# Kernel optimization log

Measured on AMD Instinct MI355X. Metric: run time of the kernel, lower is better.

The kernel has to match this reference:

```python
import jax, jax.numpy as jnp
import numpy as np

N_QUBITS = 4
N_LAYERS = 3
DIM = 2 ** N_QUBITS  # 16


def _apply_1q_const(state, U, w):
    # state: (B, 16) complex64; U: (2, 2) constant gate on wire w (wire 0 = most significant)
    B = state.shape[0]
    left, right = 2 ** w, 2 ** (N_QUBITS - w - 1)
    s = state.reshape(B, left, 2, right)
    s = jnp.einsum('ij,bajc->baic', U, s)
    return s.reshape(B, DIM)


def _apply_1q_batched(state, U, w):
    # U: (B, 2, 2) per-sample gate (data re-uploading RY angles)
    B = state.shape[0]
    left, right = 2 ** w, 2 ** (N_QUBITS - w - 1)
    s = state.reshape(B, left, 2, right)
    s = jnp.einsum('bij,bajc->baic', U, s)
    return s.reshape(B, DIM)


def _cnot(state, c, t):
    # flip target axis amplitudes where control == 1
    B = state.shape[0]
    s = state.reshape((B,) + (2,) * N_QUBITS)
    s = jnp.moveaxis(s, (1 + c, 1 + t), (N_QUBITS - 1, N_QUBITS))
    s = s.at[..., 1, :].set(s[..., 1, ::-1])
    s = jnp.moveaxis(s, (N_QUBITS - 1, N_QUBITS), (1 + c, 1 + t))
    return s.reshape(B, DIM)


def _ry_batched(theta):
    # (B,) -> (B, 2, 2) RY matrices (real, cast to complex)
    c, s = jnp.cos(theta / 2), jnp.sin(theta / 2)
    return jnp.stack([jnp.stack([c, -s], -1), jnp.stack([s, c], -1)], -2).astype(jnp.complex64)


def _rot(phi, theta, omega):
    # PennyLane Rot = RZ(omega) RY(theta) RZ(phi)
    c, s = jnp.cos(theta / 2), jnp.sin(theta / 2)
    row0 = jnp.stack([jnp.exp(-1j * (phi + omega) / 2) * c, -jnp.exp(1j * (phi - omega) / 2) * s])
    row1 = jnp.stack([jnp.exp(-1j * (phi - omega) / 2) * s, jnp.exp(1j * (phi + omega) / 2) * c])
    return jnp.stack([row0, row1]).astype(jnp.complex64)


def _circuit(angles, q_weights):
    # angles: (B, 4); q_weights: (3, 4, 3). Returns <Z_0> per sample, (B,)
    B = angles.shape[0]
    state = jnp.zeros((B, DIM), jnp.complex64).at[:, 0].set(1.0)
    for l in range(N_LAYERS):
        # AngleEmbedding(rotation='Y') — same inputs re-uploaded each layer
        for w in range(N_QUBITS):
            state = _apply_1q_batched(state, _ry_batched(angles[:, w]), w)
        # StronglyEntanglingLayers, single layer -> range r = 1
        for w in range(N_QUBITS):
            phi, theta, omega = q_weights[l, w, 0], q_weights[l, w, 1], q_weights[l, w, 2]
            state = _apply_1q_const(state, _rot(phi, theta, omega), w)
        for w in range(N_QUBITS):
            state = _cnot(state, w, (w + 1) % N_QUBITS)
    probs = jnp.abs(state.reshape(B, 2, DIM // 2)) ** 2
    return jnp.sum(probs[:, 0, :], -1) - jnp.sum(probs[:, 1, :], -1)


def setup_inputs() -> dict:
    key = jax.random.key(0)
    k0, k1, k2, k3 = jax.random.split(key, 4)
    N, H = 800000, 128
    edge_attr = jax.random.normal(k0, (N, H), dtype=jnp.float32)
    W_proj = jax.random.normal(k1, (N_QUBITS, H), dtype=jnp.float32) / np.sqrt(H)
    b_proj = jax.random.normal(k2, (N_QUBITS,), dtype=jnp.float32) * 0.01
    # TorchLayer default init: Uniform(0, 2*pi)
    q_weights = jax.random.uniform(k3, (N_LAYERS, N_QUBITS, 3), dtype=jnp.float32) * (2 * np.pi)
    return {"edge_attr": edge_attr, "W_proj": W_proj, "b_proj": b_proj, "q_weights": q_weights}


def reference(edge_attr, W_proj, b_proj, q_weights):
    q_in = jnp.tanh(edge_attr @ W_proj.T + b_proj) * jnp.pi  # (N, 4)
    z = _circuit(q_in, q_weights)                            # (N,)
    return jax.nn.sigmoid(z).reshape(-1, 1)
```

## Files before the change

kernel.cpp:

```cpp
#include <hip/hip_runtime.h>

#define NQ  4
#define DIM 16
#define NL  3
#define HD  128

__global__ __launch_bounds__(256) void rqa_kernel(
    const float* __restrict__ edge,
    const float* __restrict__ W,
    const float* __restrict__ b,
    const float* __restrict__ qw,
    float* __restrict__ out, int N)
{
    __shared__ float rotm[NL * NQ][4];

    const int tid = threadIdx.x;
    if (tid < NL * NQ) {
        float phi = qw[tid * 3 + 0];
        float th  = qw[tid * 3 + 1];
        float om  = qw[tid * 3 + 2];
        float ct, st, ca, sa, cb, sb;
        sincosf(0.5f * th, &st, &ct);
        sincosf(0.5f * (phi + om), &sa, &ca);
        sincosf(0.5f * (phi - om), &sb, &cb);
        rotm[tid][0] =  ca * ct;
        rotm[tid][1] = -sa * ct;
        rotm[tid][2] = -cb * st;
        rotm[tid][3] = -sb * st;
    }
    __syncthreads();

    const int gid = blockIdx.x * 256 + tid;
    if (gid >= N) return;

    const float4* __restrict__ row = (const float4*)(edge + (size_t)gid * HD);
    float acc[NQ];
    #pragma unroll
    for (int o = 0; o < NQ; ++o) acc[o] = b[o];
    #pragma unroll 8
    for (int i = 0; i < HD / 4; ++i) {
        float4 x = row[i];
        #pragma unroll
        for (int o = 0; o < NQ; ++o) {
            acc[o] += x.x * W[o * HD + 4 * i + 0]
                    + x.y * W[o * HD + 4 * i + 1]
                    + x.z * W[o * HD + 4 * i + 2]
                    + x.w * W[o * HD + 4 * i + 3];
        }
    }

    const float PIF = 3.14159265358979323846f;
    float cy[NQ], sy[NQ];
    #pragma unroll
    for (int w = 0; w < NQ; ++w) {
        float a = PIF * tanhf(acc[w]);
        sincosf(0.5f * a, &sy[w], &cy[w]);
    }

    float sr[DIM], si[DIM];
    #pragma unroll
    for (int n = 0; n < DIM; ++n) { sr[n] = 0.f; si[n] = 0.f; }
    sr[0] = 1.f;

    for (int l = 0; l < NL; ++l) {
        #pragma unroll
        for (int w = 0; w < NQ; ++w) {
            const int str = 1 << (3 - w);
            const float c = cy[w], s = sy[w];
            #pragma unroll
            for (int i0 = 0; i0 < DIM; ++i0) {
                if (i0 & str) continue;
                const int i1 = i0 | str;
                float r0 = c * sr[i0] - s * sr[i1];
                float m0 = c * si[i0] - s * si[i1];
                float r1 = s * sr[i0] + c * sr[i1];
                float m1 = s * si[i0] + c * si[i1];
                sr[i0] = r0; si[i0] = m0; sr[i1] = r1; si[i1] = m1;
            }
        }
        #pragma unroll
        for (int w = 0; w < NQ; ++w) {
            const float ar = rotm[l * NQ + w][0];
            const float ai = rotm[l * NQ + w][1];
            const float br = rotm[l * NQ + w][2];
            const float bi = rotm[l * NQ + w][3];
            const int str = 1 << (3 - w);
            #pragma unroll
            for (int i0 = 0; i0 < DIM; ++i0) {
                if (i0 & str) continue;
                const int i1 = i0 | str;
                const float s0r = sr[i0], s0i = si[i0];
                const float s1r = sr[i1], s1i = si[i1];
                sr[i0] =  ar * s0r - ai * s0i + br * s1r - bi * s1i;
                si[i0] =  ar * s0i + ai * s0r + br * s1i + bi * s1r;
                sr[i1] = -br * s0r - bi * s0i + ar * s1r + ai * s1i;
                si[i1] = -br * s0i + bi * s0r + ar * s1i - ai * s1r;
            }
        }
        #pragma unroll
        for (int w = 0; w < NQ; ++w) {
            const int cb_ = 1 << (3 - w);
            const int tb_ = 1 << (3 - ((w + 1) & 3));
            #pragma unroll
            for (int n = 0; n < DIM; ++n) {
                if ((n & cb_) && !(n & tb_)) {
                    const int m = n | tb_;
                    float t0 = sr[n]; sr[n] = sr[m]; sr[m] = t0;
                    float t1 = si[n]; si[n] = si[m]; si[m] = t1;
                }
            }
        }
    }

    float z = 0.f;
    #pragma unroll
    for (int n = 0; n < DIM; ++n) {
        const float p = sr[n] * sr[n] + si[n] * si[n];
        z = (n < 8) ? (z + p) : (z - p);
    }
    out[gid] = 1.0f / (1.0f + expf(-z));
}

extern "C" void kernel_launch(void* const* d_in, const int* in_sizes, int n_in,
                              void* d_out, int out_size, void* d_ws, size_t ws_size,
                              hipStream_t stream) {
    const float* edge = (const float*)d_in[0];
    const float* W    = (const float*)d_in[1];
    const float* b    = (const float*)d_in[2];
    const float* qw   = (const float*)d_in[3];
    float* out = (float*)d_out;

    const int N = in_sizes[0] / HD;
    const int blocks = (N + 255) / 256;
    rqa_kernel<<<dim3(blocks), dim3(256), 0, stream>>>(edge, W, b, qw, out, N);
}
```

Measured before the change: 118.4 us.

## Cooperatively load edge rows with 4 lanes per row for coalesced projection

The projection GEMV is restructured so that each group of 4 lanes cooperatively reads one 512-byte row with interleaved float4 loads, reduces partial sums with shuffles, and stages the 4 projected values per row in shared memory. Previously each thread streamed its own row, which produced strided, uncoalesced accesses across a wavefront. The quantum simulation part is unchanged and reads its inputs from shared memory after a barrier. This adds shuffle work and a shared-memory round trip in exchange for far better global-memory coalescing on a bandwidth-bound read of about 400 MB.

```diff
diff --git a/kernel.cpp b/kernel.cpp
--- a/kernel.cpp
+++ b/kernel.cpp
@@ -13,6 +13,7 @@
     float* __restrict__ out, int N)
 {
     __shared__ float rotm[NL * NQ][4];
+    __shared__ float4 accs[256];
 
     const int tid = threadIdx.x;
     if (tid < NL * NQ) {
@@ -28,26 +29,50 @@
         rotm[tid][2] = -cb * st;
         rotm[tid][3] = -sb * st;
     }
+
+    const int wid  = tid >> 6;
+    const int lane = tid & 63;
+    const int sub  = lane & 3;
+    const int rgrp = lane >> 2;
+
+    const size_t blockRow0 = (size_t)blockIdx.x * 256;
+    const float4* __restrict__ Wv = (const float4*)W;
+
+    #pragma unroll
+    for (int p = 0; p < 4; ++p) {
+        const int local = wid * 64 + p * 16 + rgrp;
+        const size_t r = blockRow0 + local;
+        float a0 = 0.f, a1 = 0.f, a2 = 0.f, a3 = 0.f;
+        if (r < (size_t)N) {
+            const float4* __restrict__ row = (const float4*)(edge + r * HD);
+            #pragma unroll
+            for (int j = 0; j < 8; ++j) {
+                const int c4 = sub + 4 * j;
+                float4 x  = row[c4];
+                float4 w0 = Wv[0 * 32 + c4];
+                float4 w1 = Wv[1 * 32 + c4];
+                float4 w2 = Wv[2 * 32 + c4];
+                float4 w3 = Wv[3 * 32 + c4];
+                a0 += x.x * w0.x + x.y * w0.y + x.z * w0.z + x.w * w0.w;
+                a1 += x.x * w1.x + x.y * w1.y + x.z * w1.z + x.w * w1.w;
+                a2 += x.x * w2.x + x.y * w2.y + x.z * w2.z + x.w * w2.w;
+                a3 += x.x * w3.x + x.y * w3.y + x.z * w3.z + x.w * w3.w;
+            }
+        }
+        a0 += __shfl_xor(a0, 1); a0 += __shfl_xor(a0, 2);
+        a1 += __shfl_xor(a1, 1); a1 += __shfl_xor(a1, 2);
+        a2 += __shfl_xor(a2, 1); a2 += __shfl_xor(a2, 2);
+        a3 += __shfl_xor(a3, 1); a3 += __shfl_xor(a3, 2);
+        if (sub == 0)
+            accs[local] = make_float4(a0 + b[0], a1 + b[1], a2 + b[2], a3 + b[3]);
+    }
     __syncthreads();
 
-    const int gid = blockIdx.x * 256 + tid;
-    if (gid >= N) return;
+    const size_t gid = blockRow0 + tid;
+    if (gid >= (size_t)N) return;
 
-    const float4* __restrict__ row = (const float4*)(edge + (size_t)gid * HD);
-    float acc[NQ];
-    #pragma unroll
-    for (int o = 0; o < NQ; ++o) acc[o] = b[o];
-    #pragma unroll 8
-    for (int i = 0; i < HD / 4; ++i) {
-        float4 x = row[i];
-        #pragma unroll
-        for (int o = 0; o < NQ; ++o) {
-            acc[o] += x.x * W[o * HD + 4 * i + 0]
-                    + x.y * W[o * HD + 4 * i + 1]
-                    + x.z * W[o * HD + 4 * i + 2]
-                    + x.w * W[o * HD + 4 * i + 3];
-        }
-    }
+    const float4 accv = accs[tid];
+    float acc[NQ] = {accv.x, accv.y, accv.z, accv.w};
 
     const float PIF = 3.14159265358979323846f;
     float cy[NQ], sy[NQ];
```

Result: slower. 154.4 us (+30.4%).

## Persistent multi-row threads that overlap next-row loads with the circuit sim, plus RY/Rot gate fusion

Applied to the files above, without the earlier changes.

Launches a fixed grid of 1024 blocks in which each thread processes 4 rows strided by the grid size. The next row's edge_attr chunks are loaded and its projection accumulated between the layers of the current row's state-vector simulation, so memory latency overlaps with the arithmetic. The per-sample RY gate and the constant Rot gate on each wire are folded into one 2x2 complex matrix, which roughly halves the gate-application work. Occupancy is pinned via launch_bounds. Coverage now depends on N fitting within 1024*256*4 rows, so larger inputs would leave rows uncomputed.

```diff
diff --git a/kernel.cpp b/kernel.cpp
--- a/kernel.cpp
+++ b/kernel.cpp
@@ -1,18 +1,22 @@
 #include <hip/hip_runtime.h>
 
-#define NQ  4
-#define DIM 16
-#define NL  3
-#define HD  128
-
-__global__ __launch_bounds__(256) void rqa_kernel(
+#define NQ    4
+#define DIM   16
+#define NL    3
+#define HD    128
+#define KROWS 4
+#define NTHR  256
+#define NBLK  1024
+#define PIF   3.14159265358979323846f
+
+__global__ __launch_bounds__(NTHR, 4) void rqa_kernel(
     const float* __restrict__ edge,
     const float* __restrict__ W,
     const float* __restrict__ b,
     const float* __restrict__ qw,
     float* __restrict__ out, int N)
 {
-    __shared__ float rotm[NL * NQ][4];
+    __shared__ float4 rotm4[NL * NQ];
 
     const int tid = threadIdx.x;
     if (tid < NL * NQ) {
@@ -23,102 +27,184 @@
         sincosf(0.5f * th, &st, &ct);
         sincosf(0.5f * (phi + om), &sa, &ca);
         sincosf(0.5f * (phi - om), &sb, &cb);
-        rotm[tid][0] =  ca * ct;
-        rotm[tid][1] = -sa * ct;
-        rotm[tid][2] = -cb * st;
-        rotm[tid][3] = -sb * st;
+        rotm4[tid] = make_float4(ca * ct, -sa * ct, -cb * st, -sb * st);
     }
     __syncthreads();
 
-    const int gid = blockIdx.x * 256 + tid;
-    if (gid >= N) return;
-
-    const float4* __restrict__ row = (const float4*)(edge + (size_t)gid * HD);
-    float acc[NQ];
-    #pragma unroll
-    for (int o = 0; o < NQ; ++o) acc[o] = b[o];
-    #pragma unroll 8
-    for (int i = 0; i < HD / 4; ++i) {
-        float4 x = row[i];
-        #pragma unroll
-        for (int o = 0; o < NQ; ++o) {
-            acc[o] += x.x * W[o * HD + 4 * i + 0]
-                    + x.y * W[o * HD + 4 * i + 1]
-                    + x.z * W[o * HD + 4 * i + 2]
-                    + x.w * W[o * HD + 4 * i + 3];
-        }
-    }
-
-    const float PIF = 3.14159265358979323846f;
-    float cy[NQ], sy[NQ];
-    #pragma unroll
-    for (int w = 0; w < NQ; ++w) {
-        float a = PIF * tanhf(acc[w]);
-        sincosf(0.5f * a, &sy[w], &cy[w]);
-    }
-
-    float sr[DIM], si[DIM];
-    #pragma unroll
-    for (int n = 0; n < DIM; ++n) { sr[n] = 0.f; si[n] = 0.f; }
-    sr[0] = 1.f;
-
-    for (int l = 0; l < NL; ++l) {
+    const unsigned G  = NBLK * NTHR;
+    const unsigned Nu = (unsigned)N;
+    unsigned r = blockIdx.x * NTHR + tid;
+
+    float4 x[8];
+    float acc[NQ], nacc[NQ];
+
+    {
+        const unsigned rc = r < Nu ? r : Nu - 1;
+        const float4* __restrict__ rowp = (const float4*)(edge + (size_t)rc * HD);
+        #pragma unroll
+        for (int o = 0; o < NQ; ++o) nacc[o] = 0.f;
+        #pragma unroll
+        for (int q = 0; q < 4; ++q) {
+            #pragma unroll
+            for (int j = 0; j < 8; ++j) x[j] = rowp[q * 8 + j];
+            #pragma unroll
+            for (int j = 0; j < 8; ++j) {
+                const int c0 = q * 32 + j * 4;
+                #pragma unroll
+                for (int o = 0; o < NQ; ++o)
+                    nacc[o] += x[j].x * W[o*HD + c0 + 0] + x[j].y * W[o*HD + c0 + 1]
+                             + x[j].z * W[o*HD + c0 + 2] + x[j].w * W[o*HD + c0 + 3];
+            }
+        }
+        #pragma unroll
+        for (int o = 0; o < NQ; ++o) acc[o] = nacc[o];
+    }
+
+    #pragma unroll 1
+    for (int k = 1; k < KROWS; ++k) {
+        const unsigned rn  = r + G;
+        const unsigned rnc = rn < Nu ? rn : Nu - 1;
+        const float4* __restrict__ rowp = (const float4*)(edge + (size_t)rnc * HD);
+
+        #pragma unroll
+        for (int j = 0; j < 8; ++j) x[j] = rowp[j];
+
+        float cy[NQ], sy[NQ];
         #pragma unroll
         for (int w = 0; w < NQ; ++w) {
-            const int str = 1 << (3 - w);
-            const float c = cy[w], s = sy[w];
-            #pragma unroll
-            for (int i0 = 0; i0 < DIM; ++i0) {
-                if (i0 & str) continue;
-                const int i1 = i0 | str;
-                float r0 = c * sr[i0] - s * sr[i1];
-                float m0 = c * si[i0] - s * si[i1];
-                float r1 = s * sr[i0] + c * sr[i1];
-                float m1 = s * si[i0] + c * si[i1];
-                sr[i0] = r0; si[i0] = m0; sr[i1] = r1; si[i1] = m1;
-            }
-        }
+            float a = PIF * tanhf(acc[w] + b[w]);
+            sincosf(0.5f * a, &sy[w], &cy[w]);
+        }
+        float sr[DIM], si[DIM];
+        #pragma unroll
+        for (int n = 0; n < DIM; ++n) { sr[n] = 0.f; si[n] = 0.f; }
+        sr[0] = 1.f;
+        #pragma unroll
+        for (int o = 0; o < NQ; ++o) nacc[o] = 0.f;
+
+        #pragma unroll
+        for (int l = 0; l < NL; ++l) {
+            #pragma unroll
+            for (int w = 0; w < NQ; ++w) {
+                const float4 g = rotm4[l * 4 + w];
+                const float c = cy[w], s = sy[w];
+                const float m0r = g.x * c + g.z * s;
+                const float m0i = g.y * c + g.w * s;
+                const float m1r = g.z * c - g.x * s;
+                const float m1i = g.w * c - g.y * s;
+                const int str = 1 << (3 - w);
+                #pragma unroll
+                for (int i0 = 0; i0 < DIM; ++i0) {
+                    if (i0 & str) continue;
+                    const int i1 = i0 | str;
+                    const float s0r = sr[i0], s0i = si[i0], s1r = sr[i1], s1i = si[i1];
+                    sr[i0] =  m0r*s0r - m0i*s0i + m1r*s1r - m1i*s1i;
+                    si[i0] =  m0r*s0i + m0i*s0r + m1r*s1i + m1i*s1r;
+                    sr[i1] = -m1r*s0r - m1i*s0i + m0r*s1r + m0i*s1i;
+                    si[i1] = -m1r*s0i + m1i*s0r + m0r*s1i - m0i*s1r;
+                }
+            }
+            #pragma unroll
+            for (int w = 0; w < NQ; ++w) {
+                const int cb_ = 1 << (3 - w);
+                const int tb_ = 1 << (3 - ((w + 1) & 3));
+                #pragma unroll
+                for (int n = 0; n < DIM; ++n) {
+                    if ((n & cb_) && !(n & tb_)) {
+                        const int m = n | tb_;
+                        float t0 = sr[n]; sr[n] = sr[m]; sr[m] = t0;
+                        float t1 = si[n]; si[n] = si[m]; si[m] = t1;
+                    }
+                }
+            }
+            #pragma unroll
+            for (int j = 0; j < 8; ++j) {
+                const int c0 = l * 32 + j * 4;
+                #pragma unroll
+                for (int o = 0; o < NQ; ++o)
+                    nacc[o] += x[j].x * W[o*HD + c0 + 0] + x[j].y * W[o*HD + c0 + 1]
+                             + x[j].z * W[o*HD + c0 + 2] + x[j].w * W[o*HD + c0 + 3];
+            }
+            #pragma unroll
+            for (int j = 0; j < 8; ++j) x[j] = rowp[(l + 1) * 8 + j];
+        }
+
+        float z = 0.f;
+        #pragma unroll
+        for (int n = 0; n < DIM; ++n) {
+            const float p = sr[n]*sr[n] + si[n]*si[n];
+            z = (n < 8) ? (z + p) : (z - p);
+        }
+        if (r < Nu) out[r] = 1.f / (1.f + expf(-z));
+
+        #pragma unroll
+        for (int j = 0; j < 8; ++j) {
+            const int c0 = 96 + j * 4;
+            #pragma unroll
+            for (int o = 0; o < NQ; ++o)
+                nacc[o] += x[j].x * W[o*HD + c0 + 0] + x[j].y * W[o*HD + c0 + 1]
+                         + x[j].z * W[o*HD + c0 + 2] + x[j].w * W[o*HD + c0 + 3];
+        }
+        #pragma unroll
+        for (int o = 0; o < NQ; ++o) acc[o] = nacc[o];
+        r = rn;
+    }
+
+    {
+        float cy[NQ], sy[NQ];
         #pragma unroll
         for (int w = 0; w < NQ; ++w) {
-            const float ar = rotm[l * NQ + w][0];
-            const float ai = rotm[l * NQ + w][1];
-            const float br = rotm[l * NQ + w][2];
-            const float bi = rotm[l * NQ + w][3];
-            const int str = 1 << (3 - w);
-            #pragma unroll
-            for (int i0 = 0; i0 < DIM; ++i0) {
-                if (i0 & str) continue;
-                const int i1 = i0 | str;
-                const float s0r = sr[i0], s0i = si[i0];
-                const float s1r = sr[i1], s1i = si[i1];
-                sr[i0] =  ar * s0r - ai * s0i + br * s1r - bi * s1i;
-                si[i0] =  ar * s0i + ai * s0r + br * s1i + bi * s1r;
-                sr[i1] = -br * s0r - bi * s0i + ar * s1r + ai * s1i;
-                si[i1] = -br * s0i + bi * s0r + ar * s1i - ai * s1r;
-            }
-        }
-        #pragma unroll
-        for (int w = 0; w < NQ; ++w) {
-            const int cb_ = 1 << (3 - w);
-            const int tb_ = 1 << (3 - ((w + 1) & 3));
-            #pragma unroll
-            for (int n = 0; n < DIM; ++n) {
-                if ((n & cb_) && !(n & tb_)) {
-                    const int m = n | tb_;
-                    float t0 = sr[n]; sr[n] = sr[m]; sr[m] = t0;
-                    float t1 = si[n]; si[n] = si[m]; si[m] = t1;
-                }
-            }
-        }
-    }
-
-    float z = 0.f;
-    #pragma unroll
-    for (int n = 0; n < DIM; ++n) {
-        const float p = sr[n] * sr[n] + si[n] * si[n];
-        z = (n < 8) ? (z + p) : (z - p);
-    }
-    out[gid] = 1.0f / (1.0f + expf(-z));
+            float a = PIF * tanhf(acc[w] + b[w]);
+            sincosf(0.5f * a, &sy[w], &cy[w]);
+        }
+        float sr[DIM], si[DIM];
+        #pragma unroll
+        for (int n = 0; n < DIM; ++n) { sr[n] = 0.f; si[n] = 0.f; }
+        sr[0] = 1.f;
+        #pragma unroll
+        for (int l = 0; l < NL; ++l) {
+            #pragma unroll
+            for (int w = 0; w < NQ; ++w) {
+                const float4 g = rotm4[l * 4 + w];
+                const float c = cy[w], s = sy[w];
+                const float m0r = g.x * c + g.z * s;
+                const float m0i = g.y * c + g.w * s;
+                const float m1r = g.z * c - g.x * s;
+                const float m1i = g.w * c - g.y * s;
+                const int str = 1 << (3 - w);
+                #pragma unroll
+                for (int i0 = 0; i0 < DIM; ++i0) {
+                    if (i0 & str) continue;
+                    const int i1 = i0 | str;
+                    const float s0r = sr[i0], s0i = si[i0], s1r = sr[i1], s1i = si[i1];
+                    sr[i0] =  m0r*s0r - m0i*s0i + m1r*s1r - m1i*s1i;
+                    si[i0] =  m0r*s0i + m0i*s0r + m1r*s1i + m1i*s1r;
+                    sr[i1] = -m1r*s0r - m1i*s0i + m0r*s1r + m0i*s1i;
+                    si[i1] = -m1r*s0i + m1i*s0r + m0r*s1i - m0i*s1r;
+                }
+            }
+            #pragma unroll
+            for (int w = 0; w < NQ; ++w) {
+                const int cb_ = 1 << (3 - w);
+                const int tb_ = 1 << (3 - ((w + 1) & 3));
+                #pragma unroll
+                for (int n = 0; n < DIM; ++n) {
+                    if ((n & cb_) && !(n & tb_)) {
+                        const int m = n | tb_;
+                        float t0 = sr[n]; sr[n] = sr[m]; sr[m] = t0;
+                        float t1 = si[n]; si[n] = si[m]; si[m] = t1;
+                    }
+                }
+            }
+        }
+        float z = 0.f;
+        #pragma unroll
+        for (int n = 0; n < DIM; ++n) {
+            const float p = sr[n]*sr[n] + si[n]*si[n];
+            z = (n < 8) ? (z + p) : (z - p);
+        }
+        if (r < Nu) out[r] = 1.f / (1.f + expf(-z));
+    }
 }
 
 extern "C" void kernel_launch(void* const* d_in, const int* in_sizes, int n_in,
@@ -131,6 +217,5 @@
     float* out = (float*)d_out;
 
     const int N = in_sizes[0] / HD;
-    const int blocks = (N + 255) / 256;
-    rqa_kernel<<<dim3(blocks), dim3(256), 0, stream>>>(edge, W, b, qw, out, N);
+    rqa_kernel<<<dim3(NBLK), dim3(NTHR), 0, stream>>>(edge, W, b, qw, out, N);
 }
```

After: 446.1 us. +276.8%, slower.
